# Kernel optimization log

Hardware: AMD Instinct MI355X
Metric: run time of the kernel (lower is better)

## Reference

```python
import jax, jax.numpy as jnp
import numpy as np

D_IN = 1024
D_OUT = 1024
N_HEADS = 16
HEAD_DIM = D_OUT // N_HEADS


def setup_inputs() -> dict:
    key = jax.random.key(0)
    ks = jax.random.split(key, 6)
    s = 0.02
    x = jax.random.normal(ks[0], (4, 2048, D_IN), dtype=jnp.float32)
    Wq = jax.random.normal(ks[1], (D_IN, D_OUT), dtype=jnp.float32) * s
    Wk = jax.random.normal(ks[2], (D_IN, D_OUT), dtype=jnp.float32) * s
    Wv = jax.random.normal(ks[3], (D_IN, D_OUT), dtype=jnp.float32) * s
    Wo = jax.random.normal(ks[4], (D_OUT, D_OUT), dtype=jnp.float32) * s
    bo = jax.random.normal(ks[5], (D_OUT,), dtype=jnp.float32) * s
    return {"x": x, "Wq": Wq, "Wk": Wk, "Wv": Wv, "Wo": Wo, "bo": bo}


def reference(x, Wq, Wk, Wv, Wo, bo):
    B, S, _ = x.shape
    # projections -> [B, H, S, Dh]
    def split_heads(t):
        return t.reshape(B, S, N_HEADS, HEAD_DIM).transpose(0, 2, 1, 3)
    q = split_heads(x @ Wq)
    k = split_heads(x @ Wk)
    v = split_heads(x @ Wv)
    scores = jnp.einsum('bhqd,bhkd->bhqk', q, k)  # [B,H,S,S]
    causal = jnp.triu(jnp.ones((S, S), dtype=bool), k=1)
    scores = jnp.where(causal, -jnp.inf, scores)
    attn = jax.nn.softmax(scores / np.sqrt(HEAD_DIM).astype(np.float32), axis=-1)
    ctx = jnp.einsum('bhqk,bhkd->bhqd', attn, v)  # [B,H,S,Dh]
    ctx = ctx.transpose(0, 2, 1, 3).reshape(B, S, D_OUT)
    return ctx @ Wo + bo
```

## Files before the change

### kernel.cpp

```cpp
#include <hip/hip_runtime.h>
#include <hip/hip_bf16.h>
#include <math.h>

typedef __attribute__((ext_vector_type(8))) short bf16x8;
typedef __attribute__((ext_vector_type(4))) float f32x4;
typedef __attribute__((ext_vector_type(16))) float f32x16;
typedef __attribute__((ext_vector_type(4))) unsigned int u32x4;

static constexpr int Mtot = 8192;
static constexpr int Dmod = 1024;
static constexpr int SEQ  = 2048;
static constexpr int NH   = 16;
static constexpr int DH   = 64;

static constexpr float QSCALE = 0.18033688011112042f;

__device__ __forceinline__ unsigned short f2bf(float x) {
    unsigned int u = __float_as_uint(x);
    u += 0x7fff + ((u >> 16) & 1);
    return (unsigned short)(u >> 16);
}

__device__ __forceinline__ void gload_lds16(const void* g, void* l) {
    __builtin_amdgcn_global_load_lds(
        (const __attribute__((address_space(1))) unsigned int*)g,
        (__attribute__((address_space(3))) unsigned int*)l, 16, 0, 0);
}

__global__ __launch_bounds__(256)
void cvt_bf16(const float* __restrict__ in, unsigned short* __restrict__ out, int n4) {
    int i = blockIdx.x * blockDim.x + threadIdx.x;
    const int stride = gridDim.x * blockDim.x;
    for (; i < n4; i += stride) {
        float4 v = ((const float4*)in)[i];
        ushort4 o;
        o.x = f2bf(v.x); o.y = f2bf(v.y); o.z = f2bf(v.z); o.w = f2bf(v.w);
        ((ushort4*)out)[i] = o;
    }
}

__global__ __launch_bounds__(256)
void transpose_cvt4(const float* __restrict__ W0, const float* __restrict__ W1,
                    const float* __restrict__ W2, const float* __restrict__ W3,
                    unsigned short* __restrict__ T0, unsigned short* __restrict__ T1,
                    unsigned short* __restrict__ T2, unsigned short* __restrict__ T3) {
    __shared__ float tile[64][68];
    const int z = blockIdx.z;
    const float* W = z == 0 ? W0 : z == 1 ? W1 : z == 2 ? W2 : W3;
    unsigned short* Wt = z == 0 ? T0 : z == 1 ? T1 : z == 2 ? T2 : T3;

    const int n0 = blockIdx.x * 64, k0 = blockIdx.y * 64;
    const int t = threadIdx.x;
    const int r = t >> 4, c4 = (t & 15) * 4;
#pragma unroll
    for (int i = 0; i < 4; ++i) {
        float4 v = *(const float4*)&W[(size_t)(k0 + r + i * 16) * Dmod + n0 + c4];
        tile[c4 + 0][r + i * 16] = v.x;
        tile[c4 + 1][r + i * 16] = v.y;
        tile[c4 + 2][r + i * 16] = v.z;
        tile[c4 + 3][r + i * 16] = v.w;
    }
    __syncthreads();
#pragma unroll
    for (int i = 0; i < 4; ++i) {
        ushort4 o;
        o.x = f2bf(tile[r + i * 16][c4 + 0]);
        o.y = f2bf(tile[r + i * 16][c4 + 1]);
        o.z = f2bf(tile[r + i * 16][c4 + 2]);
        o.w = f2bf(tile[r + i * 16][c4 + 3]);
        *(ushort4*)&Wt[(size_t)(n0 + r + i * 16) * Dmod + k0 + c4] = o;
    }
}

__device__ __forceinline__ void gemm_core(const unsigned short* __restrict__ A,
                                          const unsigned short* __restrict__ Wt,
                                          int m0, int n0, int K,
                                          short* As, short* Bs, f32x4 acc[4][4]) {
    const int t   = threadIdx.x;
    const int wid = t >> 6, l = t & 63;
    const int wr  = wid >> 1, wc = wid & 1;
    const int r16 = l & 15, g = l >> 4;
    const int srow = t >> 2;
    const int scol = (t & 3) * 8;

    for (int k0 = 0; k0 < K; k0 += 32) {
        __syncthreads();
#pragma unroll
        for (int c = 0; c < 2; ++c) {
            gload_lds16(A  + (size_t)(m0 + c * 64 + srow) * K + k0 + scol,
                        (char*)As + c * 4096 + wid * 1024);
            gload_lds16(Wt + (size_t)(n0 + c * 64 + srow) * K + k0 + scol,
                        (char*)Bs + c * 4096 + wid * 1024);
        }
        __syncthreads();
        bf16x8 af[4], bv[4];
#pragma unroll
        for (int mi = 0; mi < 4; ++mi)
            af[mi] = *(const bf16x8*)&As[(wr * 64 + mi * 16 + r16) * 32 + g * 8];
#pragma unroll
        for (int ni = 0; ni < 4; ++ni)
            bv[ni] = *(const bf16x8*)&Bs[(wc * 64 + ni * 16 + r16) * 32 + g * 8];
#pragma unroll
        for (int mi = 0; mi < 4; ++mi)
#pragma unroll
            for (int ni = 0; ni < 4; ++ni)
                acc[mi][ni] = __builtin_amdgcn_mfma_f32_16x16x32_bf16(
                    af[mi], bv[ni], acc[mi][ni], 0, 0, 0);
    }
}

__global__ __launch_bounds__(256)
void qkv_gemm(const unsigned short* __restrict__ xb,
              const unsigned short* __restrict__ wtq,
              const unsigned short* __restrict__ wtk,
              const unsigned short* __restrict__ wtv,
              unsigned short* __restrict__ Qb,
              unsigned short* __restrict__ Kb,
              unsigned short* __restrict__ Vtb) {
    __shared__ __align__(16) short As[128 * 32];
    __shared__ __align__(16) short Bs[128 * 32];
    const int region = blockIdx.x >> 3;
    const int n0 = (blockIdx.x & 7) * 128;
    const int m0 = blockIdx.y * 128;
    const unsigned short* Wt = region == 0 ? wtq : (region == 1 ? wtk : wtv);

    f32x4 acc[4][4];
    const f32x4 z = {0.f, 0.f, 0.f, 0.f};
#pragma unroll
    for (int i = 0; i < 4; ++i)
#pragma unroll
        for (int j = 0; j < 4; ++j) acc[i][j] = z;

    gemm_core(xb, Wt, m0, n0, Dmod, As, Bs, acc);

    const int t = threadIdx.x, wid = t >> 6, l = t & 63;
    const int wr = wid >> 1, wc = wid & 1, r16 = l & 15, g = l >> 4;

    if (region <= 1) {
        unsigned short* out = region ? Kb : Qb;
        const float qs = region == 0 ? QSCALE : 1.0f;
#pragma unroll
        for (int mi = 0; mi < 4; ++mi) {
            const int mrow = m0 + wr * 64 + mi * 16 + g * 4;
#pragma unroll
            for (int ni = 0; ni < 4; ++ni) {
                const int ncol = n0 + wc * 64 + ni * 16 + r16;
#pragma unroll
                for (int reg = 0; reg < 4; ++reg)
                    out[(size_t)(mrow + reg) * Dmod + ncol] = f2bf(acc[mi][ni][reg] * qs);
            }
        }
    } else {
#pragma unroll
        for (int mi = 0; mi < 4; ++mi) {
            const int mrow = m0 + wr * 64 + mi * 16 + g * 4;
            const int b = mrow >> 11, s = mrow & 2047;
#pragma unroll
            for (int ni = 0; ni < 4; ++ni) {
                const int n = n0 + wc * 64 + ni * 16 + r16;
                const int bh = b * NH + (n >> 6), d = n & 63;
                ushort4 o;
                o.x = f2bf(acc[mi][ni][0]); o.y = f2bf(acc[mi][ni][1]);
                o.z = f2bf(acc[mi][ni][2]); o.w = f2bf(acc[mi][ni][3]);
                *(ushort4*)&Vtb[((size_t)bh * DH + d) * SEQ + s] = o;
            }
        }
    }
}

__global__ __launch_bounds__(256)
void out_gemm(const unsigned short* __restrict__ Cx,
              const unsigned short* __restrict__ wto,
              const float* __restrict__ bias,
              float* __restrict__ out) {
    __shared__ __align__(16) short As[128 * 32];
    __shared__ __align__(16) short Bs[128 * 32];
    const int n0 = blockIdx.x * 128, m0 = blockIdx.y * 128;

    f32x4 acc[4][4];
    const f32x4 z = {0.f, 0.f, 0.f, 0.f};
#pragma unroll
    for (int i = 0; i < 4; ++i)
#pragma unroll
        for (int j = 0; j < 4; ++j) acc[i][j] = z;

    gemm_core(Cx, wto, m0, n0, Dmod, As, Bs, acc);

    const int t = threadIdx.x, wid = t >> 6, l = t & 63;
    const int wr = wid >> 1, wc = wid & 1, r16 = l & 15, g = l >> 4;
    float bv[4];
#pragma unroll
    for (int ni = 0; ni < 4; ++ni) bv[ni] = bias[n0 + wc * 64 + ni * 16 + r16];
#pragma unroll
    for (int mi = 0; mi < 4; ++mi) {
        const int mrow = m0 + wr * 64 + mi * 16 + g * 4;
#pragma unroll
        for (int ni = 0; ni < 4; ++ni) {
            const int ncol = n0 + wc * 64 + ni * 16 + r16;
#pragma unroll
            for (int reg = 0; reg < 4; ++reg)
                out[(size_t)(mrow + reg) * Dmod + ncol] = acc[mi][ni][reg] + bv[ni];
        }
    }
}

__global__ __launch_bounds__(256, 2)
void attn_mfma(const unsigned short* __restrict__ Qg,
               const unsigned short* __restrict__ Kg,
               const unsigned short* __restrict__ Vtg,
               unsigned short* __restrict__ Ctx) {
    __shared__ __align__(16) short Ks[2][64 * 64];
    __shared__ __align__(16) short Vs[2][64 * 64];
    __shared__ float sm[4][32];

    const int id   = blockIdx.x;
    const int bh   = ((id >> 6) << 3) | (id & 7);
    const int pidx = (id >> 3) & 7;
    const int b = bh >> 4, h = bh & 15;
    const int t = threadIdx.x, wid = t >> 6, l = t & 63;
    const int lo = l & 31, hi = l >> 5;
    const int srow8 = t >> 3, scolb = (t & 7) * 16;

    auto stageKV = [&](int jt, int buf) {
        const int k0s = jt * 64;
#pragma unroll
        for (int c = 0; c < 2; ++c) {
            const int row = c * 32 + srow8;
            const int swz = scolb ^ ((row & 7) << 4);
            gload_lds16((const char*)Kg + ((size_t)(b * SEQ + k0s + row) * Dmod + h * DH) * 2 + swz,
                        (char*)&Ks[buf][0] + c * 4096 + wid * 1024);
            gload_lds16((const char*)Vtg + ((size_t)(bh * DH + row) * SEQ + k0s) * 2 + swz,
                        (char*)&Vs[buf][0] + c * 4096 + wid * 1024);
        }
    };

    int cur = 0;
    for (int pass = 0; pass < 2; ++pass) {
        const int qt = pass ? pidx : 15 - pidx;
        const int q0 = qt * 128;
        const int qw0 = q0 + wid * 32;
        const int qg = qw0 + lo;

        bf16x8 bq[4];
#pragma unroll
        for (int dc = 0; dc < 4; ++dc)
            bq[dc] = *(const bf16x8*)&Qg[(size_t)(b * SEQ + qg) * Dmod + h * DH + dc * 16 + 8 * hi];

        stageKV(0, cur);

        float m_run = -1e30f, l_run = 0.f;
        f32x16 oacc[2];
#pragma unroll
        for (int nb = 0; nb < 2; ++nb)
#pragma unroll
            for (int r = 0; r < 16; ++r) oacc[nb][r] = 0.f;

        __syncthreads();

        const int jmax = 2 * qt + 1;
        for (int jt = 0; jt <= jmax; ++jt) {
            if (jt < jmax) stageKV(jt + 1, cur ^ 1);
            const char* Kc = (const char*)&Ks[cur][0];
            const char* Vc = (const char*)&Vs[cur][0];
            const bool diag = (jt >= 2 * qt);

#pragma unroll
            for (int c32 = 0; c32 < 2; ++c32) {
                const int krow = c32 * 32 + lo;
                const int kswz = (krow & 7) << 4;
                bf16x8 ak[4];
#pragma unroll
                for (int dc = 0; dc < 4; ++dc)
                    ak[dc] = *(const bf16x8*)(Kc + krow * 128 + ((dc * 32 + 16 * hi) ^ kswz));
                f32x16 st;
#pragma unroll
                for (int r = 0; r < 16; ++r) st[r] = 0.f;
                __builtin_amdgcn_s_setprio(1);
#pragma unroll
                for (int dc = 0; dc < 4; ++dc)
                    st = __builtin_amdgcn_mfma_f32_32x32x16_bf16(ak[dc], bq[dc], st, 0, 0, 0);
                __builtin_amdgcn_s_setprio(0);

                if (diag) {
                    const int kvb = jt * 64 + c32 * 32 + 4 * hi;
#pragma unroll
                    for (int r = 0; r < 16; ++r) {
                        const int kvg = kvb + (r & 3) + 8 * (r >> 2);
                        if (kvg > qg) st[r] = -1e30f;
                    }
                }

                float pmax = st[0];
#pragma unroll
                for (int r = 1; r < 16; ++r) pmax = fmaxf(pmax, st[r]);
                pmax = fmaxf(pmax, __shfl_xor(pmax, 32));

                if (!__all(pmax <= m_run + 8.f)) {
                    const float mnew = fmaxf(m_run, pmax);
                    const float sc = exp2f(m_run - mnew);
                    l_run *= sc;
                    m_run = mnew;
                    if (l < 32) sm[wid][lo] = sc;
                    asm volatile("s_waitcnt lgkmcnt(0)" ::: "memory");
#pragma unroll
                    for (int rq = 0; rq < 4; ++rq) {
                        const f32x4 s4 = *(const f32x4*)&sm[wid][8 * rq + 4 * hi];
#pragma unroll
                        for (int e = 0; e < 4; ++e) {
                            oacc[0][rq * 4 + e] *= s4[e];
                            oacc[1][rq * 4 + e] *= s4[e];
                        }
                    }
                }

                float p[16];
                float rsum = 0.f;
#pragma unroll
                for (int r = 0; r < 16; ++r) { p[r] = exp2f(st[r] - m_run); rsum += p[r]; }
                rsum += __shfl_xor(rsum, 32);
                l_run += rsum;

#pragma unroll
                for (int kb = 0; kb < 2; ++kb) {
                    unsigned int x, zz, y, w;
                    asm("v_cvt_pk_bf16_f32 %0, %1, %2" : "=v"(x)  : "v"(p[kb*8+0]), "v"(p[kb*8+1]));
                    asm("v_cvt_pk_bf16_f32 %0, %1, %2" : "=v"(zz) : "v"(p[kb*8+2]), "v"(p[kb*8+3]));
                    asm("v_cvt_pk_bf16_f32 %0, %1, %2" : "=v"(y)  : "v"(p[kb*8+4]), "v"(p[kb*8+5]));
                    asm("v_cvt_pk_bf16_f32 %0, %1, %2" : "=v"(w)  : "v"(p[kb*8+6]), "v"(p[kb*8+7]));
                    asm volatile("v_permlane32_swap_b32 %0, %1" : "+v"(x),  "+v"(y));
                    asm volatile("v_permlane32_swap_b32 %0, %1" : "+v"(zz), "+v"(w));
                    u32x4 aw; aw[0] = x; aw[1] = zz; aw[2] = y; aw[3] = w;
                    const bf16x8 paf = __builtin_bit_cast(bf16x8, aw);

                    const int vbyte = c32 * 64 + kb * 32 + 16 * hi;
                    const int row0 = lo, row1 = 32 + lo;
                    const bf16x8 vb0 = *(const bf16x8*)(Vc + row0 * 128 + (vbyte ^ ((row0 & 7) << 4)));
                    const bf16x8 vb1 = *(const bf16x8*)(Vc + row1 * 128 + (vbyte ^ ((row1 & 7) << 4)));

                    __builtin_amdgcn_s_setprio(1);
                    oacc[0] = __builtin_amdgcn_mfma_f32_32x32x16_bf16(paf, vb0, oacc[0], 0, 0, 0);
                    oacc[1] = __builtin_amdgcn_mfma_f32_32x32x16_bf16(paf, vb1, oacc[1], 0, 0, 0);
                    __builtin_amdgcn_s_setprio(0);
                }
            }
            __syncthreads();
            cur ^= 1;
        }

        if (l < 32) sm[wid][lo] = l_run;
        asm volatile("s_waitcnt lgkmcnt(0)" ::: "memory");
#pragma unroll
        for (int rq = 0; rq < 4; ++rq) {
            const f32x4 lv = *(const f32x4*)&sm[wid][8 * rq + 4 * hi];
#pragma unroll
            for (int e = 0; e < 4; ++e) {
                const float inv = 1.0f / lv[e];
                const int qrow = qw0 + 8 * rq + 4 * hi + e;
                const size_t rb = (size_t)(b * SEQ + qrow) * Dmod + h * DH + lo;
                Ctx[rb]      = f2bf(oacc[0][rq * 4 + e] * inv);
                Ctx[rb + 32] = f2bf(oacc[1][rq * 4 + e] * inv);
            }
        }
    }
}

extern "C" void kernel_launch(void* const* d_in, const int* in_sizes, int n_in,
                              void* d_out, int out_size, void* d_ws, size_t ws_size,
                              hipStream_t stream) {
    const float* x  = (const float*)d_in[0];
    const float* Wq = (const float*)d_in[1];
    const float* Wk = (const float*)d_in[2];
    const float* Wv = (const float*)d_in[3];
    const float* Wo = (const float*)d_in[4];
    const float* bo = (const float*)d_in[5];
    float* out = (float*)d_out;

    const size_t MD = (size_t)Mtot * Dmod;
    const size_t DD = (size_t)Dmod * Dmod;
    unsigned short* xb  = (unsigned short*)d_ws;
    unsigned short* wtq = xb  + MD;
    unsigned short* wtk = wtq + DD;
    unsigned short* wtv = wtk + DD;
    unsigned short* wto = wtv + DD;
    unsigned short* Qb  = wto + DD;
    unsigned short* Kb  = Qb  + MD;
    unsigned short* Vtb = Kb  + MD;
    unsigned short* Cx  = Vtb + MD;

    cvt_bf16<<<2048, 256, 0, stream>>>(x, xb, (int)(MD / 4));
    transpose_cvt4<<<dim3(16, 16, 4), 256, 0, stream>>>(Wq, Wk, Wv, Wo,
                                                        wtq, wtk, wtv, wto);

    qkv_gemm<<<dim3(24, 64), 256, 0, stream>>>(xb, wtq, wtk, wtv, Qb, Kb, Vtb);

    attn_mfma<<<512, 256, 0, stream>>>(Qb, Kb, Vtb, Cx);

    out_gemm<<<dim3(8, 64), 256, 0, stream>>>(Cx, wto, bo, out);
}
```

Measured before the change: 204.1 us.

## Replace GEMMs with 256x256-tile, double-buffered, swizzled-LDS 512-thread kernel

Replaces the 128x128 single-buffered QKV and output GEMMs with one templated 256x256-tile kernel using 8 waves, 128 KB of double-buffered LDS with XOR swizzling, and split-K staging interleaved with MFMA phases. The staging pattern uses vmcnt waits and s_setprio so global loads overlap compute. Blocks are mapped to XCDs for L2 locality. The QKV GEMM relies on wtq, wtk and wtv being contiguous so they act as one 3072-column weight matrix. The larger tiles cut global traffic per FLOP, but with only 384 and 128 blocks some CUs may sit idle, and one block per CU limits latency hiding.

```diff
diff --git a/kernel.cpp b/kernel.cpp
--- a/kernel.cpp
+++ b/kernel.cpp
@@ -72,134 +72,199 @@
     }
 }
 
-__device__ __forceinline__ void gemm_core(const unsigned short* __restrict__ A,
-                                          const unsigned short* __restrict__ Wt,
-                                          int m0, int n0, int K,
-                                          short* As, short* Bs, f32x4 acc[4][4]) {
-    const int t   = threadIdx.x;
+template<int MODE>
+__global__ __launch_bounds__(512)
+void gemm256(const unsigned short* __restrict__ A,
+             const unsigned short* __restrict__ Bw,
+             const float* __restrict__ bias,
+             unsigned short* __restrict__ Qb,
+             unsigned short* __restrict__ Kb,
+             unsigned short* __restrict__ Vtb,
+             float* __restrict__ Fout) {
+    __shared__ __align__(16) char lds[131072];
+
+    const int id  = blockIdx.x;
+    const int xcd = id & 7, idx = id >> 3;
+    constexpr int NTN = MODE == 0 ? 12 : 4;
+    const int mt = xcd * 4 + idx / NTN;
+    const int nt = idx % NTN;
+    const int m0 = mt * 256, n0 = nt * 256;
+
+    const int t = threadIdx.x;
     const int wid = t >> 6, l = t & 63;
-    const int wr  = wid >> 1, wc = wid & 1;
+    const int wm = wid >> 2, wn = wid & 3;
     const int r16 = l & 15, g = l >> 4;
-    const int srow = t >> 2;
-    const int scol = (t & 3) * 8;
-
-    for (int k0 = 0; k0 < K; k0 += 32) {
-        __syncthreads();
-#pragma unroll
-        for (int c = 0; c < 2; ++c) {
-            gload_lds16(A  + (size_t)(m0 + c * 64 + srow) * K + k0 + scol,
-                        (char*)As + c * 4096 + wid * 1024);
-            gload_lds16(Wt + (size_t)(n0 + c * 64 + srow) * K + k0 + scol,
-                        (char*)Bs + c * 4096 + wid * 1024);
-        }
-        __syncthreads();
-        bf16x8 af[4], bv[4];
-#pragma unroll
-        for (int mi = 0; mi < 4; ++mi)
-            af[mi] = *(const bf16x8*)&As[(wr * 64 + mi * 16 + r16) * 32 + g * 8];
-#pragma unroll
-        for (int ni = 0; ni < 4; ++ni)
-            bv[ni] = *(const bf16x8*)&Bs[(wc * 64 + ni * 16 + r16) * 32 + g * 8];
-#pragma unroll
-        for (int mi = 0; mi < 4; ++mi)
-#pragma unroll
-            for (int ni = 0; ni < 4; ++ni)
+
+    auto stage = [&](const unsigned short* src, int row0, int kt, int kh, int regionOff) {
+        char* dst = lds + regionOff + wid * 1024;
+#pragma unroll
+        for (int r = 0; r < 2; ++r) {
+            const int o  = r * 8192 + t * 16;
+            const int lg = o ^ (((o >> 7) & 3) << 4);
+            gload_lds16((const char*)src + (size_t)(row0 + (lg >> 6)) * 2048
+                            + kt * 128 + kh * 64 + (lg & 63),
+                        dst + r * 8192);
+        }
+    };
+
+    f32x4 acc[8][4];
+    const f32x4 z = {0.f, 0.f, 0.f, 0.f};
+#pragma unroll
+    for (int i = 0; i < 8; ++i)
+#pragma unroll
+        for (int j = 0; j < 4; ++j) acc[i][j] = z;
+
+    stage(A,  m0, 0, 0, 0);
+    stage(Bw, n0, 0, 0, 16384);
+    stage(A,  m0, 0, 1, 32768);
+    stage(Bw, n0, 0, 1, 49152);
+
+    const int arow0 = wm * 128 + r16;
+    const int brow0 = wn * 64 + r16;
+    const int gb = g * 16;
+
+    for (int kt = 0; kt < 16; ++kt) {
+        const int buf  = (kt & 1) << 16;
+        const int nbuf = buf ^ 65536;
+        const int ktn  = kt < 15 ? kt + 1 : 15;
+        bf16x8 af[8], bv[2];
+
+        stage(A, m0, ktn, 0, nbuf);
+        asm volatile("s_waitcnt vmcnt(6)" ::: "memory");
+        __builtin_amdgcn_s_barrier();
+#pragma unroll
+        for (int mi = 0; mi < 8; ++mi) {
+            const int row = arow0 + mi * 16;
+            af[mi] = *(const bf16x8*)(lds + buf
+                      + ((row * 64 + gb) ^ (((row >> 1) & 3) << 4)));
+        }
+#pragma unroll
+        for (int ni = 0; ni < 2; ++ni) {
+            const int row = brow0 + ni * 16;
+            bv[ni] = *(const bf16x8*)(lds + buf + 16384
+                      + ((row * 64 + gb) ^ (((row >> 1) & 3) << 4)));
+        }
+        asm volatile("s_waitcnt lgkmcnt(0)" ::: "memory");
+        __builtin_amdgcn_sched_barrier(0);
+        __builtin_amdgcn_s_setprio(1);
+#pragma unroll
+        for (int mi = 0; mi < 8; ++mi)
+#pragma unroll
+            for (int ni = 0; ni < 2; ++ni)
                 acc[mi][ni] = __builtin_amdgcn_mfma_f32_16x16x32_bf16(
                     af[mi], bv[ni], acc[mi][ni], 0, 0, 0);
-    }
-}
-
-__global__ __launch_bounds__(256)
-void qkv_gemm(const unsigned short* __restrict__ xb,
-              const unsigned short* __restrict__ wtq,
-              const unsigned short* __restrict__ wtk,
-              const unsigned short* __restrict__ wtv,
-              unsigned short* __restrict__ Qb,
-              unsigned short* __restrict__ Kb,
-              unsigned short* __restrict__ Vtb) {
-    __shared__ __align__(16) short As[128 * 32];
-    __shared__ __align__(16) short Bs[128 * 32];
-    const int region = blockIdx.x >> 3;
-    const int n0 = (blockIdx.x & 7) * 128;
-    const int m0 = blockIdx.y * 128;
-    const unsigned short* Wt = region == 0 ? wtq : (region == 1 ? wtk : wtv);
-
-    f32x4 acc[4][4];
-    const f32x4 z = {0.f, 0.f, 0.f, 0.f};
-#pragma unroll
-    for (int i = 0; i < 4; ++i)
-#pragma unroll
-        for (int j = 0; j < 4; ++j) acc[i][j] = z;
-
-    gemm_core(xb, Wt, m0, n0, Dmod, As, Bs, acc);
-
-    const int t = threadIdx.x, wid = t >> 6, l = t & 63;
-    const int wr = wid >> 1, wc = wid & 1, r16 = l & 15, g = l >> 4;
-
-    if (region <= 1) {
-        unsigned short* out = region ? Kb : Qb;
-        const float qs = region == 0 ? QSCALE : 1.0f;
-#pragma unroll
-        for (int mi = 0; mi < 4; ++mi) {
-            const int mrow = m0 + wr * 64 + mi * 16 + g * 4;
+        __builtin_amdgcn_s_setprio(0);
+
+        stage(Bw, n0, ktn, 0, nbuf + 16384);
+#pragma unroll
+        for (int ni = 0; ni < 2; ++ni) {
+            const int row = brow0 + (2 + ni) * 16;
+            bv[ni] = *(const bf16x8*)(lds + buf + 16384
+                      + ((row * 64 + gb) ^ (((row >> 1) & 3) << 4)));
+        }
+        asm volatile("s_waitcnt lgkmcnt(0)" ::: "memory");
+        __builtin_amdgcn_sched_barrier(0);
+        __builtin_amdgcn_s_setprio(1);
+#pragma unroll
+        for (int mi = 0; mi < 8; ++mi)
+#pragma unroll
+            for (int ni = 0; ni < 2; ++ni)
+                acc[mi][2 + ni] = __builtin_amdgcn_mfma_f32_16x16x32_bf16(
+                    af[mi], bv[ni], acc[mi][2 + ni], 0, 0, 0);
+        __builtin_amdgcn_s_setprio(0);
+
+        stage(A, m0, ktn, 1, nbuf + 32768);
+        asm volatile("s_waitcnt vmcnt(6)" ::: "memory");
+        __builtin_amdgcn_s_barrier();
+#pragma unroll
+        for (int mi = 0; mi < 8; ++mi) {
+            const int row = arow0 + mi * 16;
+            af[mi] = *(const bf16x8*)(lds + buf + 32768
+                      + ((row * 64 + gb) ^ (((row >> 1) & 3) << 4)));
+        }
+#pragma unroll
+        for (int ni = 0; ni < 2; ++ni) {
+            const int row = brow0 + ni * 16;
+            bv[ni] = *(const bf16x8*)(lds + buf + 49152
+                      + ((row * 64 + gb) ^ (((row >> 1) & 3) << 4)));
+        }
+        asm volatile("s_waitcnt lgkmcnt(0)" ::: "memory");
+        __builtin_amdgcn_sched_barrier(0);
+        __builtin_amdgcn_s_setprio(1);
+#pragma unroll
+        for (int mi = 0; mi < 8; ++mi)
+#pragma unroll
+            for (int ni = 0; ni < 2; ++ni)
+                acc[mi][ni] = __builtin_amdgcn_mfma_f32_16x16x32_bf16(
+                    af[mi], bv[ni], acc[mi][ni], 0, 0, 0);
+        __builtin_amdgcn_s_setprio(0);
+
+        stage(Bw, n0, ktn, 1, nbuf + 49152);
+#pragma unroll
+        for (int ni = 0; ni < 2; ++ni) {
+            const int row = brow0 + (2 + ni) * 16;
+            bv[ni] = *(const bf16x8*)(lds + buf + 49152
+                      + ((row * 64 + gb) ^ (((row >> 1) & 3) << 4)));
+        }
+        asm volatile("s_waitcnt lgkmcnt(0)" ::: "memory");
+        __builtin_amdgcn_sched_barrier(0);
+        __builtin_amdgcn_s_setprio(1);
+#pragma unroll
+        for (int mi = 0; mi < 8; ++mi)
+#pragma unroll
+            for (int ni = 0; ni < 2; ++ni)
+                acc[mi][2 + ni] = __builtin_amdgcn_mfma_f32_16x16x32_bf16(
+                    af[mi], bv[ni], acc[mi][2 + ni], 0, 0, 0);
+        __builtin_amdgcn_s_setprio(0);
+    }
+
+    if constexpr (MODE == 0) {
+        const int region = n0 >> 10;
+        if (region <= 1) {
+            unsigned short* outp = region ? Kb : Qb;
+            const float qs = region == 0 ? QSCALE : 1.0f;
+#pragma unroll
+            for (int mi = 0; mi < 8; ++mi) {
+                const int mrow = m0 + wm * 128 + mi * 16 + g * 4;
+#pragma unroll
+                for (int ni = 0; ni < 4; ++ni) {
+                    const int ncol = (n0 & 1023) + wn * 64 + ni * 16 + r16;
+#pragma unroll
+                    for (int reg = 0; reg < 4; ++reg)
+                        outp[(size_t)(mrow + reg) * Dmod + ncol] = f2bf(acc[mi][ni][reg] * qs);
+                }
+            }
+        } else {
+#pragma unroll
+            for (int mi = 0; mi < 8; ++mi) {
+                const int mrow = m0 + wm * 128 + mi * 16 + g * 4;
+                const int bidx = mrow >> 11, s = mrow & 2047;
+#pragma unroll
+                for (int ni = 0; ni < 4; ++ni) {
+                    const int n = (n0 & 1023) + wn * 64 + ni * 16 + r16;
+                    const int bh = bidx * NH + (n >> 6), d = n & 63;
+                    ushort4 o;
+                    o.x = f2bf(acc[mi][ni][0]); o.y = f2bf(acc[mi][ni][1]);
+                    o.z = f2bf(acc[mi][ni][2]); o.w = f2bf(acc[mi][ni][3]);
+                    *(ushort4*)&Vtb[((size_t)bh * DH + d) * SEQ + s] = o;
+                }
+            }
+        }
+    } else {
+        float bb[4];
+#pragma unroll
+        for (int ni = 0; ni < 4; ++ni)
+            bb[ni] = bias[n0 + wn * 64 + ni * 16 + r16];
+#pragma unroll
+        for (int mi = 0; mi < 8; ++mi) {
+            const int mrow = m0 + wm * 128 + mi * 16 + g * 4;
 #pragma unroll
             for (int ni = 0; ni < 4; ++ni) {
-                const int ncol = n0 + wc * 64 + ni * 16 + r16;
+                const int ncol = n0 + wn * 64 + ni * 16 + r16;
 #pragma unroll
                 for (int reg = 0; reg < 4; ++reg)
-                    out[(size_t)(mrow + reg) * Dmod + ncol] = f2bf(acc[mi][ni][reg] * qs);
+                    Fout[(size_t)(mrow + reg) * Dmod + ncol] = acc[mi][ni][reg] + bb[ni];
             }
-        }
-    } else {
-#pragma unroll
-        for (int mi = 0; mi < 4; ++mi) {
-            const int mrow = m0 + wr * 64 + mi * 16 + g * 4;
-            const int b = mrow >> 11, s = mrow & 2047;
-#pragma unroll
-            for (int ni = 0; ni < 4; ++ni) {
-                const int n = n0 + wc * 64 + ni * 16 + r16;
-                const int bh = b * NH + (n >> 6), d = n & 63;
-                ushort4 o;
-                o.x = f2bf(acc[mi][ni][0]); o.y = f2bf(acc[mi][ni][1]);
-                o.z = f2bf(acc[mi][ni][2]); o.w = f2bf(acc[mi][ni][3]);
-                *(ushort4*)&Vtb[((size_t)bh * DH + d) * SEQ + s] = o;
-            }
-        }
-    }
-}
-
-__global__ __launch_bounds__(256)
-void out_gemm(const unsigned short* __restrict__ Cx,
-              const unsigned short* __restrict__ wto,
-              const float* __restrict__ bias,
-              float* __restrict__ out) {
-    __shared__ __align__(16) short As[128 * 32];
-    __shared__ __align__(16) short Bs[128 * 32];
-    const int n0 = blockIdx.x * 128, m0 = blockIdx.y * 128;
-
-    f32x4 acc[4][4];
-    const f32x4 z = {0.f, 0.f, 0.f, 0.f};
-#pragma unroll
-    for (int i = 0; i < 4; ++i)
-#pragma unroll
-        for (int j = 0; j < 4; ++j) acc[i][j] = z;
-
-    gemm_core(Cx, wto, m0, n0, Dmod, As, Bs, acc);
-
-    const int t = threadIdx.x, wid = t >> 6, l = t & 63;
-    const int wr = wid >> 1, wc = wid & 1, r16 = l & 15, g = l >> 4;
-    float bv[4];
-#pragma unroll
-    for (int ni = 0; ni < 4; ++ni) bv[ni] = bias[n0 + wc * 64 + ni * 16 + r16];
-#pragma unroll
-    for (int mi = 0; mi < 4; ++mi) {
-        const int mrow = m0 + wr * 64 + mi * 16 + g * 4;
-#pragma unroll
-        for (int ni = 0; ni < 4; ++ni) {
-            const int ncol = n0 + wc * 64 + ni * 16 + r16;
-#pragma unroll
-            for (int reg = 0; reg < 4; ++reg)
-                out[(size_t)(mrow + reg) * Dmod + ncol] = acc[mi][ni][reg] + bv[ni];
         }
     }
 }
@@ -391,9 +456,9 @@
     transpose_cvt4<<<dim3(16, 16, 4), 256, 0, stream>>>(Wq, Wk, Wv, Wo,
                                                         wtq, wtk, wtv, wto);
 
-    qkv_gemm<<<dim3(24, 64), 256, 0, stream>>>(xb, wtq, wtk, wtv, Qb, Kb, Vtb);
+    gemm256<0><<<384, 512, 0, stream>>>(xb, wtq, nullptr, Qb, Kb, Vtb, nullptr);
 
     attn_mfma<<<512, 256, 0, stream>>>(Qb, Kb, Vtb, Cx);
 
-    out_gemm<<<dim3(8, 64), 256, 0, stream>>>(Cx, wto, bo, out);
-}
+    gemm256<1><<<128, 512, 0, stream>>>(Cx, wto, bo, nullptr, nullptr, nullptr, out);
+}
```

Result: faster. 190.6 us (-6.6%).
